# Kernel tuning notes

Hardware: AMD Instinct MI355X
Metric: run time of the kernel (lower is better)

The kernel has to match this reference:

```python
import jax, jax.numpy as jnp
import numpy as np

EPS = 1e-6

def _rms_norm(t, g):
    # t: [B, S, C] (applied before the view to heads, matching the torch code)
    y = t.astype(jnp.float32)
    y = jax.lax.rsqrt(jnp.mean(y * y, axis=-1, keepdims=True) + EPS)
    return (t * y * g).astype(t.dtype)

def _apply_rope(t, cos, sin):
    # t: [B, S, N, D]; cos/sin: [1, S, 1, D//2]; interleaved pair rotation
    b, s, n, d = t.shape
    tr = t.reshape(b, s, n, d // 2, 2)
    tre, tim = tr[..., 0], tr[..., 1]
    out = jnp.stack([tre * cos - tim * sin, tre * sin + tim * cos], axis=-1)
    return out.reshape(b, s, n, d)

def setup_inputs() -> dict:
    key = jax.random.key(0)
    ks = jax.random.split(key, 8)
    B, S, DIM, N, D = 2, 1024, 3072, 24, 128
    x = jax.random.normal(ks[0], (B, S, DIM), dtype=jnp.float32)
    seq_lens = jax.random.randint(ks[1], (B,), S // 2, S + 1, dtype=jnp.int32)
    grid_sizes = jnp.tile(jnp.array([[16, 8, 8]], dtype=jnp.int32), (B, 1))
    # rope angle table [1024, D//2]: pos * inv_freq
    inv_freq = 1.0 / (10000.0 ** (jnp.arange(D // 2, dtype=jnp.float32) * 2.0 / D))
    freqs = jnp.arange(1024, dtype=jnp.float32)[:, None] * inv_freq[None, :]
    sc = 1.0 / np.sqrt(DIM)
    Wq = jax.random.normal(ks[2], (DIM, DIM), dtype=jnp.float32) * sc
    Wk = jax.random.normal(ks[3], (DIM, DIM), dtype=jnp.float32) * sc
    Wv = jax.random.normal(ks[4], (DIM, DIM), dtype=jnp.float32) * sc
    Wo = jax.random.normal(ks[5], (DIM, DIM), dtype=jnp.float32) * sc
    bq = jnp.zeros((DIM,), jnp.float32); bk = jnp.zeros((DIM,), jnp.float32)
    bv = jnp.zeros((DIM,), jnp.float32); bo = jnp.zeros((DIM,), jnp.float32)
    gq = jnp.ones((DIM,), jnp.float32); gk = jnp.ones((DIM,), jnp.float32)
    return {"x": x, "seq_lens": seq_lens, "grid_sizes": grid_sizes, "freqs": freqs,
            "Wq": Wq, "bq": bq, "Wk": Wk, "bk": bk, "Wv": Wv, "bv": bv,
            "Wo": Wo, "bo": bo, "gq": gq, "gk": gk}

def reference(x, seq_lens, grid_sizes, freqs, Wq, bq, Wk, bk, Wv, bv, Wo, bo, gq, gk):
    b, s, dim = x.shape
    d = 2 * freqs.shape[1]          # head_dim
    n = dim // d                    # num_heads
    q = _rms_norm(x @ Wq.T + bq, gq).reshape(b, s, n, d)
    k = _rms_norm(x @ Wk.T + bk, gk).reshape(b, s, n, d)
    v = (x @ Wv.T + bv).reshape(b, s, n, d)
    ang = freqs[:s]                 # [S, D//2]
    cos = jnp.cos(ang)[None, :, None, :]
    sin = jnp.sin(ang)[None, :, None, :]
    q = _apply_rope(q, cos, sin)
    k = _apply_rope(k, cos, sin)
    # full attention (window_size = (-1,-1)), varlen key masking via seq_lens
    scale = d ** -0.5
    scores = jnp.einsum('bind,bjnd->bnij', q, k) * scale   # [B,N,S,S]
    key_valid = jnp.arange(s)[None, :] < seq_lens[:, None]  # [B,S]
    scores = jnp.where(key_valid[:, None, None, :], scores, jnp.finfo(scores.dtype).min)
    p = jax.nn.softmax(scores, axis=-1)
    out = jnp.einsum('bnij,bjnd->bind', p, v).reshape(b, s, dim)
    return out @ Wo.T + bo
```

## Files before the change

kernel.cpp:

```cpp
#include <hip/hip_runtime.h>
#include <cmath>

#define BB   2
#define SS   1024
#define DIMM 3072
#define NHH  24
#define HDD  128
#define MM   (BB * SS)

typedef _Float16 f16;
typedef __attribute__((ext_vector_type(8))) _Float16 half8;
typedef __attribute__((ext_vector_type(4))) float floatx4;
typedef unsigned int u32;
typedef const __attribute__((address_space(1))) u32* gp1;
typedef __attribute__((address_space(3))) u32* lp3;

__device__ __forceinline__ void gload_lds16(const void* g, void* l) {
    __builtin_amdgcn_global_load_lds((gp1)g, (lp3)l, 16, 0, 0);
}

__global__ __launch_bounds__(256) void cvt_f16_kernel(
    const float* __restrict__ in, f16* __restrict__ outp, int n8)
{
    int i = blockIdx.x * 256 + threadIdx.x;
    if (i >= n8) return;
    const float4* p = (const float4*)(in + (size_t)i * 8);
    float4 a = p[0], b = p[1];
    half8 h = {(f16)a.x, (f16)a.y, (f16)a.z, (f16)a.w,
               (f16)b.x, (f16)b.y, (f16)b.z, (f16)b.w};
    *(half8*)(outp + (size_t)i * 8) = h;
}

__global__ __launch_bounds__(256) void cvt3_f16_kernel(
    const float* __restrict__ w0, const float* __restrict__ w1,
    const float* __restrict__ w2, f16* __restrict__ outp, int n8each)
{
    int i = blockIdx.x * 256 + threadIdx.x;
    int sel = i / n8each;
    int j = i - sel * n8each;
    const float* in = sel == 0 ? w0 : (sel == 1 ? w1 : w2);
    const float4* p = (const float4*)(in + (size_t)j * 8);
    float4 a = p[0], b = p[1];
    half8 h = {(f16)a.x, (f16)a.y, (f16)a.z, (f16)a.w,
               (f16)b.x, (f16)b.y, (f16)b.z, (f16)b.w};
    *(half8*)(outp + (size_t)i * 8) = h;
}

__global__ __launch_bounds__(256) void cvt5_f16_kernel(
    const float* __restrict__ x,
    const float* __restrict__ w0, const float* __restrict__ w1,
    const float* __restrict__ w2, const float* __restrict__ w3,
    f16* __restrict__ outx, f16* __restrict__ outw, int n8x, int n8each)
{
    int i = blockIdx.x * 256 + threadIdx.x;
    const float* src;
    f16* op;
    if (i < n8x) {
        src = x + (size_t)i * 8;
        op  = outx + (size_t)i * 8;
    } else {
        int k = i - n8x;
        int sel = k / n8each;
        int j = k - sel * n8each;
        const float* in = sel == 0 ? w0 : (sel == 1 ? w1 : (sel == 2 ? w2 : w3));
        src = in + (size_t)j * 8;
        op  = outw + (size_t)k * 8;
    }
    const float4* p = (const float4*)src;
    float4 a = p[0], b = p[1];
    half8 h = {(f16)a.x, (f16)a.y, (f16)a.z, (f16)a.w,
               (f16)b.x, (f16)b.y, (f16)b.z, (f16)b.w};
    *(half8*)op = h;
}

template<bool QKV>
__global__ __launch_bounds__(256) void gemm_p32(
    const f16* __restrict__ A,
    const f16* __restrict__ W0, const f16* __restrict__ W1, const f16* __restrict__ W2,
    const float* __restrict__ b0, const float* __restrict__ b1, const float* __restrict__ b2,
    f16* __restrict__ D0, f16* __restrict__ D1, f16* __restrict__ D2,
    float* __restrict__ F, const int* __restrict__ seq)
{
    constexpr int K = DIMM;
    constexpr int NSTEP = K / 32;
    constexpr int TS = 128 * 32;
    __shared__ __align__(16) f16 As[3][TS];
    __shared__ __align__(16) f16 Bs[3][TS];

    const int tid  = threadIdx.x;
    const int lane = tid & 63;
    const int wave = tid >> 6;
    const int wm = wave >> 1, wn = wave & 1;
    const int lr = lane & 15;
    const int lq = lane >> 4;

    const int id  = blockIdx.x;
    const int cpx = (int)gridDim.x >> 3;
    const int swz = (id & 7) * cpx + (id >> 3);
    const int bm = (swz & 15) << 7;
    const int bn = (swz >> 4) << 7;

    const f16* Wh; const float* bias; f16* D = nullptr;
    int nloc = bn;
    if constexpr (QKV) {
        int sel = bn / DIMM;
        nloc = bn - sel * DIMM;
        Wh   = sel == 0 ? W0 : (sel == 1 ? W1 : W2);
        bias = sel == 0 ? b0 : (sel == 1 ? b1 : b2);
        D    = sel == 0 ? D0 : (sel == 1 ? D1 : D2);
        if (sel > 0) {
            const int batch  = bm >> 10;
            const int sstart = bm & 1023;
            if (sstart >= seq[batch]) return;
        }
    } else { Wh = W0; bias = b0; }

    const int r0 = tid >> 2;
    const int g0 = ((tid & 3) ^ ((r0 >> 1) & 3)) << 3;
    const int r1 = (tid + 256) >> 2;
    const int g1 = ((tid & 3) ^ ((r1 >> 1) & 3)) << 3;
    const f16* a0  = A  + (size_t)(bm   + r0) * K + g0;
    const f16* a1  = A  + (size_t)(bm   + r1) * K + g1;
    const f16* w0p = Wh + (size_t)(nloc + r0) * K + g0;
    const f16* w1p = Wh + (size_t)(nloc + r1) * K + g1;

    auto STAGE = [&](int t, int buf) {
        const int k0 = t * 32;
        gload_lds16(a0  + k0, &As[buf][(size_t)tid * 8]);
        gload_lds16(a1  + k0, &As[buf][(size_t)(tid + 256) * 8]);
        gload_lds16(w0p + k0, &Bs[buf][(size_t)tid * 8]);
        gload_lds16(w1p + k0, &Bs[buf][(size_t)(tid + 256) * 8]);
    };

    floatx4 acc[4][4];
#pragma unroll
    for (int i = 0; i < 4; ++i)
#pragma unroll
        for (int j = 0; j < 4; ++j) acc[i][j] = (floatx4){0.f, 0.f, 0.f, 0.f};

    auto COMPUTE = [&](int buf) {
        const f16* Ab = &As[buf][0];
        const f16* Bb = &Bs[buf][0];
        half8 af[4], bf[4];
#pragma unroll
        for (int i = 0; i < 4; ++i) {
            int ra = wm * 64 + i * 16 + lr;
            int rb = wn * 64 + i * 16 + lr;
            af[i] = *(const half8*)&Ab[ra * 32 + ((lq ^ ((ra >> 1) & 3)) << 3)];
            bf[i] = *(const half8*)&Bb[rb * 32 + ((lq ^ ((rb >> 1) & 3)) << 3)];
        }
#pragma unroll
        for (int mi = 0; mi < 4; ++mi)
#pragma unroll
            for (int ni = 0; ni < 4; ++ni)
                acc[mi][ni] = __builtin_amdgcn_mfma_f32_16x16x32_f16(af[mi], bf[ni], acc[mi][ni], 0, 0, 0);
    };

    STAGE(0, 0);
    STAGE(1, 1);
    asm volatile("s_waitcnt vmcnt(4)" ::: "memory");
    __builtin_amdgcn_s_barrier();

    int cur = 0, stg = 2;
    for (int ks = 0; ks < NSTEP; ++ks) {
        const bool more = (ks + 2 < NSTEP);
        if (more) STAGE(ks + 2, stg);
        COMPUTE(cur);
        if (more) asm volatile("s_waitcnt vmcnt(4)" ::: "memory");
        else      asm volatile("s_waitcnt vmcnt(0)" ::: "memory");
        __builtin_amdgcn_s_barrier();
        cur = (cur == 2) ? 0 : cur + 1;
        stg = (stg == 2) ? 0 : stg + 1;
    }

    const int crow0 = bm + wm * 64 + (lq << 2);
    const int ccol0 = nloc + wn * 64;
#pragma unroll
    for (int ni = 0; ni < 4; ++ni) {
        const int col = ccol0 + ni * 16 + lr;
        const float bv = bias[col];
#pragma unroll
        for (int mi = 0; mi < 4; ++mi) {
            const int row = crow0 + mi * 16;
#pragma unroll
            for (int r2 = 0; r2 < 4; ++r2) {
                if constexpr (QKV)
                    D[(size_t)(row + r2) * DIMM + col] = (f16)(acc[mi][ni][r2] + bv);
                else
                    F[(size_t)(row + r2) * DIMM + col] = acc[mi][ni][r2] + bv;
            }
        }
    }
}

template<bool QKV>
__global__ __launch_bounds__(256) void gemm_f16m(
    const f16* __restrict__ A,
    const float* __restrict__ W0, const float* __restrict__ W1, const float* __restrict__ W2,
    const float* __restrict__ b0, const float* __restrict__ b1, const float* __restrict__ b2,
    f16* __restrict__ D0, f16* __restrict__ D1, f16* __restrict__ D2,
    float* __restrict__ F)
{
    constexpr int K = DIMM;
    constexpr int NSTEP = K / 32;
    __shared__ f16 As[128 * 32];
    __shared__ f16 Bs[128 * 32];

    const int tid  = threadIdx.x;
    const int lane = tid & 63;
    const int wave = tid >> 6;
    const int wm = wave >> 1, wn = wave & 1;
    const int lr = lane & 15;
    const int lq = lane >> 4;

    const int id  = blockIdx.x;
    const int cpx = (int)gridDim.x >> 3;
    const int swz = (id & 7) * cpx + (id >> 3);
    const int bm = (swz & 15) << 7;
    const int bn = (swz >> 4) << 7;

    const float* W; const float* bias; f16* D = nullptr;
    int nloc = bn;
    if constexpr (QKV) {
        int sel = bn / DIMM;
        nloc = bn - sel * DIMM;
        W    = sel == 0 ? W0 : (sel == 1 ? W1 : W2);
        bias = sel == 0 ? b0 : (sel == 1 ? b1 : b2);
        D    = sel == 0 ? D0 : (sel == 1 ? D1 : D2);
    } else { W = W0; bias = b0; }

    const int r0 = tid >> 2;
    const int c8 = (tid & 3) << 3;
    const float* bp0 = W + (size_t)(nloc + r0) * K + c8;
    const float* bp1 = W + (size_t)(nloc + r0 + 64) * K + c8;

    const int arow_l = lane >> 2;
    const int acol_l = (lane & 3) << 3;
    const f16* agbase = A + (size_t)bm * K;

    float4 sb00, sb01, sb10, sb11;
    auto LOADB = [&](int k0) {
        sb00 = *(const float4*)(bp0 + k0); sb01 = *(const float4*)(bp0 + k0 + 4);
        sb10 = *(const float4*)(bp1 + k0); sb11 = *(const float4*)(bp1 + k0 + 4);
    };
    auto STOREB = [&]() {
        half8 h0 = {(f16)sb00.x, (f16)sb00.y, (f16)sb00.z, (f16)sb00.w,
                    (f16)sb01.x, (f16)sb01.y, (f16)sb01.z, (f16)sb01.w};
        half8 h1 = {(f16)sb10.x, (f16)sb10.y, (f16)sb10.z, (f16)sb10.w,
                    (f16)sb11.x, (f16)sb11.y, (f16)sb11.z, (f16)sb11.w};
        *(half8*)&Bs[r0 * 32 + c8]        = h0;
        *(half8*)&Bs[(r0 + 64) * 32 + c8] = h1;
    };

    floatx4 acc[4][4];
#pragma unroll
    for (int i = 0; i < 4; ++i)
#pragma unroll
        for (int j = 0; j < 4; ++j) acc[i][j] = (floatx4){0.f, 0.f, 0.f, 0.f};

    LOADB(0);
    for (int ks = 0; ks < NSTEP; ++ks) {
        const int k0 = ks * 32;
        __syncthreads();
#pragma unroll
        for (int i = 0; i < 2; ++i) {
            int rbase = wave * 32 + i * 16;
            gload_lds16(agbase + (size_t)(rbase + arow_l) * K + k0 + acol_l,
                        &As[rbase * 32]);
        }
        STOREB();
        __syncthreads();
        if (ks + 1 < NSTEP) LOADB(k0 + 32);

        half8 af[4], bf[4];
#pragma unroll
        for (int i = 0; i < 4; ++i) {
            af[i] = *(const half8*)&As[(wm * 64 + i * 16 + lr) * 32 + lq * 8];
            bf[i] = *(const half8*)&Bs[(wn * 64 + i * 16 + lr) * 32 + lq * 8];
        }
#pragma unroll
        for (int mi = 0; mi < 4; ++mi)
#pragma unroll
            for (int ni = 0; ni < 4; ++ni)
                acc[mi][ni] = __builtin_amdgcn_mfma_f32_16x16x32_f16(af[mi], bf[ni], acc[mi][ni], 0, 0, 0);
    }

    const int crow0 = bm + wm * 64 + (lq << 2);
    const int ccol0 = nloc + wn * 64;
#pragma unroll
    for (int ni = 0; ni < 4; ++ni) {
        const int col = ccol0 + ni * 16 + lr;
        const float bv = bias[col];
#pragma unroll
        for (int mi = 0; mi < 4; ++mi) {
            const int row = crow0 + mi * 16;
#pragma unroll
            for (int r2 = 0; r2 < 4; ++r2) {
                if constexpr (QKV)
                    D[(size_t)(row + r2) * DIMM + col] = (f16)(acc[mi][ni][r2] + bv);
                else
                    F[(size_t)(row + r2) * DIMM + col] = acc[mi][ni][r2] + bv;
            }
        }
    }
}

__global__ __launch_bounds__(192) void rmsnorm_rope_f16(
    f16* __restrict__ q, f16* __restrict__ k,
    const float* __restrict__ gq, const float* __restrict__ gk,
    const float* __restrict__ freqs, const int* __restrict__ seq)
{
    const int row = blockIdx.x;
    const int s = row & (SS - 1);
    if (blockIdx.y == 1 && s >= seq[row >> 10]) return;
    f16* t = (blockIdx.y == 0) ? q : k;
    const float* g = (blockIdx.y == 0) ? gq : gk;
    const int tid = threadIdx.x;
    f16* base = t + (size_t)row * DIMM + tid * 16;

    half8 v0 = *(const half8*)base;
    half8 v1 = *(const half8*)(base + 8);
    float v[16];
#pragma unroll
    for (int j = 0; j < 8; ++j) { v[j] = (float)v0[j]; v[8 + j] = (float)v1[j]; }

    float ssq = 0.f;
#pragma unroll
    for (int j = 0; j < 16; ++j) ssq += v[j] * v[j];
#pragma unroll
    for (int off = 32; off > 0; off >>= 1) ssq += __shfl_down(ssq, off, 64);
    __shared__ float red[3];
    if ((tid & 63) == 0) red[tid >> 6] = ssq;
    __syncthreads();
    float tot = red[0] + red[1] + red[2];
    float sc = rsqrtf(tot * (1.0f / (float)DIMM) + 1e-6f);

    const float* gp = g + tid * 16;
    float y[16];
#pragma unroll
    for (int j = 0; j < 16; ++j) y[j] = v[j] * sc * gp[j];

#pragma unroll
    for (int p = 0; p < 8; ++p) {
        int idx = tid * 16 + 2 * p;
        int f = (idx & 127) >> 1;
        float ang = freqs[s * 64 + f];
        float cc = cosf(ang), sn = sinf(ang);
        float e = y[2 * p], o = y[2 * p + 1];
        y[2 * p]     = e * cc - o * sn;
        y[2 * p + 1] = e * sn + o * cc;
    }
    half8 o0, o1;
#pragma unroll
    for (int j = 0; j < 8; ++j) { o0[j] = (f16)y[j]; o1[j] = (f16)y[8 + j]; }
    *(half8*)base       = o0;
    *(half8*)(base + 8) = o1;
}

__global__ __launch_bounds__(256) void flash_attn_f16(
    const f16* __restrict__ Q, const f16* __restrict__ K,
    const f16* __restrict__ V, const int* __restrict__ seq_lens,
    f16* __restrict__ O)
{
    __shared__ __align__(16) f16 QPs[64 * 128];
    __shared__ __align__(16) f16 Ks[64 * 128];
    __shared__ __align__(16) f16 Vt[128 * 64];

    const int tid  = threadIdx.x;
    const int lane = tid & 63;
    const int wave = tid >> 6;
    const int ln = lane & 15;
    const int lq = lane >> 4;
    const int i0 = blockIdx.x * 64;
    const int h  = blockIdx.y;
    const int b  = blockIdx.z;
    const int slen = seq_lens[b];
    const float scale = 0.08838834764831845f;
    const size_t gstride = NHH * HDD;

    const f16* Qg = Q + ((size_t)(b * SS + i0) * NHH + h) * HDD;
#pragma unroll
    for (int rep = 0; rep < 4; ++rep) {
        int u = tid + rep * 256;
        int r = u >> 4, d0 = (u & 15) << 3;
        half8 qv = *(const half8*)(Qg + (size_t)r * gstride + d0);
        *(half8*)(QPs + r * 128 + (d0 ^ ((r & 7) << 3))) = qv;
    }
    __syncthreads();

    half8 qfrag[4];
    {
        int rq = wave * 16 + ln;
#pragma unroll
        for (int ks = 0; ks < 4; ++ks)
            qfrag[ks] = *(const half8*)(QPs + rq * 128 + ((ks * 32 + lq * 8) ^ ((rq & 7) << 3)));
    }

    floatx4 accO[8];
#pragma unroll
    for (int dt = 0; dt < 8; ++dt) accO[dt] = (floatx4){0.f, 0.f, 0.f, 0.f};
    float mrow[4] = {-3.0e38f, -3.0e38f, -3.0e38f, -3.0e38f};
    float lrow[4] = {0.f, 0.f, 0.f, 0.f};

    const int nT = (slen + 63) >> 6;
    for (int t = 0; t < nT; ++t) {
        const int j0g = t * 64;
        __syncthreads();

        const f16* Kg = K + ((size_t)(b * SS + j0g) * NHH + h) * HDD;
#pragma unroll
        for (int rep = 0; rep < 4; ++rep) {
            int u = tid + rep * 256;
            int r = u >> 4, d0 = (u & 15) << 3;
            half8 kv = *(const half8*)(Kg + (size_t)r * gstride + d0);
            *(half8*)(Ks + r * 128 + (d0 ^ ((r & 7) << 3))) = kv;
        }
        const f16* Vg = V + ((size_t)(b * SS + j0g) * NHH + h) * HDD;
        const half8 zero8 = {(f16)0, (f16)0, (f16)0, (f16)0, (f16)0, (f16)0, (f16)0, (f16)0};
#pragma unroll
        for (int rep = 0; rep < 2; ++rep) {
            int u = tid + rep * 256;
            int jp = u & 31, j0 = jp * 2;
            int d0 = (u >> 5) << 3;
            half8 va = *(const half8*)(Vg + (size_t)j0 * gstride + d0);
            half8 vb = *(const half8*)(Vg + (size_t)(j0 + 1) * gstride + d0);
            if (j0g + j0     >= slen) va = zero8;
            if (j0g + j0 + 1 >= slen) vb = zero8;
#pragma unroll
            for (int i = 0; i < 8; ++i) {
                int d = d0 + i;
                union { f16 h[2]; u32 w; } pk;
                pk.h[0] = va[i]; pk.h[1] = vb[i];
                *(u32*)(Vt + d * 64 + (j0 ^ ((d & 7) << 3))) = pk.w;
            }
        }
        __syncthreads();

        floatx4 acc_s[4];
#pragma unroll
        for (int nt = 0; nt < 4; ++nt) {
            acc_s[nt] = (floatx4){0.f, 0.f, 0.f, 0.f};
            int rk = nt * 16 + ln;
#pragma unroll
            for (int ks = 0; ks < 4; ++ks) {
                half8 kf = *(const half8*)(Ks + rk * 128 + ((ks * 32 + lq * 8) ^ ((rk & 7) << 3)));
                acc_s[nt] = __builtin_amdgcn_mfma_f32_16x16x32_f16(qfrag[ks], kf, acc_s[nt], 0, 0, 0);
            }
        }

        float s[4][4];
#pragma unroll
        for (int nt = 0; nt < 4; ++nt) {
            int j = j0g + nt * 16 + ln;
            bool valid = (j < slen);
#pragma unroll
            for (int r = 0; r < 4; ++r)
                s[nt][r] = valid ? acc_s[nt][r] * scale : -3.0e38f;
        }
        float fct[4];
#pragma unroll
        for (int r = 0; r < 4; ++r) {
            float m4 = fmaxf(fmaxf(s[0][r], s[1][r]), fmaxf(s[2][r], s[3][r]));
            m4 = fmaxf(m4, __shfl_xor(m4, 1, 64));
            m4 = fmaxf(m4, __shfl_xor(m4, 2, 64));
            m4 = fmaxf(m4, __shfl_xor(m4, 4, 64));
            m4 = fmaxf(m4, __shfl_xor(m4, 8, 64));
            float mn = fmaxf(mrow[r], m4);
            fct[r] = __expf(mrow[r] - mn);
            mrow[r] = mn;
            float ls = 0.f;
#pragma unroll
            for (int nt = 0; nt < 4; ++nt) {
                float p = __expf(s[nt][r] - mn);
                s[nt][r] = p;
                ls += p;
            }
            ls += __shfl_xor(ls, 1, 64);
            ls += __shfl_xor(ls, 2, 64);
            ls += __shfl_xor(ls, 4, 64);
            ls += __shfl_xor(ls, 8, 64);
            lrow[r] = lrow[r] * fct[r] + ls;
        }

#pragma unroll
        for (int nt = 0; nt < 4; ++nt) {
#pragma unroll
            for (int r = 0; r < 4; ++r) {
                int rw = lq * 4 + r;
                int j = nt * 16 + ln;
                QPs[(wave * 16 + rw) * 128 + (j ^ ((rw & 7) << 3))] = (f16)s[nt][r];
            }
        }

#pragma unroll
        for (int dt = 0; dt < 8; ++dt)
#pragma unroll
            for (int r = 0; r < 4; ++r) accO[dt][r] *= fct[r];

        half8 pfrag[2];
#pragma unroll
        for (int js = 0; js < 2; ++js)
            pfrag[js] = *(const half8*)(QPs + (wave * 16 + ln) * 128 + ((js * 32 + lq * 8) ^ ((ln & 7) << 3)));
#pragma unroll
        for (int dt = 0; dt < 8; ++dt) {
            int d = dt * 16 + ln;
#pragma unroll
            for (int js = 0; js < 2; ++js) {
                half8 vf = *(const half8*)(Vt + d * 64 + ((js * 32 + lq * 8) ^ ((d & 7) << 3)));
                accO[dt] = __builtin_amdgcn_mfma_f32_16x16x32_f16(pfrag[js], vf, accO[dt], 0, 0, 0);
            }
        }
    }

    float linv[4];
#pragma unroll
    for (int r = 0; r < 4; ++r) linv[r] = 1.0f / lrow[r];
    f16* Og = O + ((size_t)(b * SS + i0) * NHH + h) * HDD;
#pragma unroll
    for (int dt = 0; dt < 8; ++dt) {
#pragma unroll
        for (int r = 0; r < 4; ++r) {
            int qr = wave * 16 + lq * 4 + r;
            int d = dt * 16 + ln;
            Og[(size_t)qr * gstride + d] = (f16)(accO[dt][r] * linv[r]);
        }
    }
}

extern "C" void kernel_launch(void* const* d_in, const int* in_sizes, int n_in,
                              void* d_out, int out_size, void* d_ws, size_t ws_size,
                              hipStream_t stream)
{
    const float* x     = (const float*)d_in[0];
    const int*   seq   = (const int*)d_in[1];
    const float* freqs = (const float*)d_in[3];
    const float* Wq    = (const float*)d_in[4];
    const float* bq    = (const float*)d_in[5];
    const float* Wk    = (const float*)d_in[6];
    const float* bk    = (const float*)d_in[7];
    const float* Wv    = (const float*)d_in[8];
    const float* bv    = (const float*)d_in[9];
    const float* Wo    = (const float*)d_in[10];
    const float* bo    = (const float*)d_in[11];
    const float* gq    = (const float*)d_in[12];
    const float* gk    = (const float*)d_in[13];

    float* out = (float*)d_out;
    const size_t MD = (size_t)MM * DIMM;
    const size_t WD = (size_t)DIMM * DIMM;

    f16* X16 = (f16*)d_ws;
    f16* q16 = X16 + MD;
    f16* k16 = X16 + 2 * MD;
    f16* v16 = (f16*)d_out;

    const int nMD8 = (int)(MD / 8);
    const int nWD8 = (int)(WD / 8);
    const size_t need1 = (3 * MD + 3 * WD) * sizeof(f16);
    const size_t need2 = (3 * MD + 4 * WD) * sizeof(f16);

    if (ws_size >= need2) {
        f16* Wq16 = X16 + 3 * MD;
        f16* Wk16 = Wq16 + WD;
        f16* Wv16 = Wk16 + WD;
        f16* Wo16 = Wv16 + WD;
        cvt5_f16_kernel<<<(nMD8 + 4 * nWD8 + 255) / 256, 256, 0, stream>>>(
            x, Wq, Wk, Wv, Wo, X16, Wq16, nMD8, nWD8);
        gemm_p32<true><<<(MM / 128) * (3 * DIMM / 128), 256, 0, stream>>>(
            X16, Wq16, Wk16, Wv16, bq, bk, bv, q16, k16, v16, nullptr, seq);
        rmsnorm_rope_f16<<<dim3(MM, 2), 192, 0, stream>>>(q16, k16, gq, gk, freqs, seq);
        flash_attn_f16<<<dim3(SS / 64, NHH, BB), 256, 0, stream>>>(q16, k16, v16, seq, X16);
        gemm_p32<false><<<(MM / 128) * (DIMM / 128), 256, 0, stream>>>(
            X16, Wo16, nullptr, nullptr, bo, nullptr, nullptr, nullptr, nullptr, nullptr, out, nullptr);
    } else if (ws_size >= need1) {
        f16* Wq16 = X16 + 3 * MD;
        f16* Wk16 = Wq16 + WD;
        f16* Wv16 = Wk16 + WD;
        f16* Wo16 = Wq16;
        cvt_f16_kernel<<<nMD8 / 256, 256, 0, stream>>>(x, X16, nMD8);
        cvt3_f16_kernel<<<3 * nWD8 / 256, 256, 0, stream>>>(Wq, Wk, Wv, Wq16, nWD8);
        gemm_p32<true><<<(MM / 128) * (3 * DIMM / 128), 256, 0, stream>>>(
            X16, Wq16, Wk16, Wv16, bq, bk, bv, q16, k16, v16, nullptr, seq);
        cvt_f16_kernel<<<nWD8 / 256, 256, 0, stream>>>(Wo, Wo16, nWD8);
        rmsnorm_rope_f16<<<dim3(MM, 2), 192, 0, stream>>>(q16, k16, gq, gk, freqs, seq);
        flash_attn_f16<<<dim3(SS / 64, NHH, BB), 256, 0, stream>>>(q16, k16, v16, seq, X16);
        gemm_p32<false><<<(MM / 128) * (DIMM / 128), 256, 0, stream>>>(
            X16, Wo16, nullptr, nullptr, bo, nullptr, nullptr, nullptr, nullptr, nullptr, out, nullptr);
    } else {
        cvt_f16_kernel<<<nMD8 / 256, 256, 0, stream>>>(x, X16, nMD8);
        gemm_f16m<true><<<(MM / 128) * (3 * DIMM / 128), 256, 0, stream>>>(
            X16, Wq, Wk, Wv, bq, bk, bv, q16, k16, v16, nullptr);
        rmsnorm_rope_f16<<<dim3(MM, 2), 192, 0, stream>>>(q16, k16, gq, gk, freqs, seq);
        flash_attn_f16<<<dim3(SS / 64, NHH, BB), 256, 0, stream>>>(q16, k16, v16, seq, X16);
        gemm_f16m<false><<<(MM / 128) * (DIMM / 128), 256, 0, stream>>>(
            X16, Wo, nullptr, nullptr, bo, nullptr, nullptr, nullptr, nullptr, nullptr, out);
    }
}
```

Baseline: 342.1 us.

## Split-K the output projection GEMM into two halves plus a reduce kernel

Replaces the single output-projection GEMM (384 tiles of 128x128) with a split-K variant that launches 768 blocks, each covering half of K. The first half writes to the output with bias and the second half writes to a float scratch buffer that reuses the Wq16 workspace. A separate kernel then adds the partial into the output. The aim is better CU occupancy on the 256-CU device, at the cost of an extra fp32 write and read of the full output plus one more kernel launch.

```diff
diff --git a/kernel.cpp b/kernel.cpp
--- a/kernel.cpp
+++ b/kernel.cpp
@@ -73,6 +73,17 @@
     *(half8*)op = h;
 }
 
+__global__ __launch_bounds__(256) void reduce_add_kernel(
+    float* __restrict__ out, const float* __restrict__ P, int n4)
+{
+    int i = blockIdx.x * 256 + threadIdx.x;
+    if (i >= n4) return;
+    float4 o = ((const float4*)out)[i];
+    float4 p = ((const float4*)P)[i];
+    o.x += p.x; o.y += p.y; o.z += p.z; o.w += p.w;
+    ((float4*)out)[i] = o;
+}
+
 template<bool QKV>
 __global__ __launch_bounds__(256) void gemm_p32(
     const f16* __restrict__ A,
@@ -189,6 +200,108 @@
                 else
                     F[(size_t)(row + r2) * DIMM + col] = acc[mi][ni][r2] + bv;
             }
+        }
+    }
+}
+
+__global__ __launch_bounds__(256) void gemm_wo_sk(
+    const f16* __restrict__ A, const f16* __restrict__ W,
+    const float* __restrict__ bias, float* __restrict__ out, float* __restrict__ P)
+{
+    constexpr int K = DIMM;
+    constexpr int KH = K / 2;
+    constexpr int NSTEP = KH / 32;
+    constexpr int TS = 128 * 32;
+    __shared__ __align__(16) f16 As[3][TS];
+    __shared__ __align__(16) f16 Bs[3][TS];
+
+    const int tid  = threadIdx.x;
+    const int lane = tid & 63;
+    const int wave = tid >> 6;
+    const int wm = wave >> 1, wn = wave & 1;
+    const int lr = lane & 15;
+    const int lq = lane >> 4;
+
+    const int id  = blockIdx.x;
+    const int cpx = (int)gridDim.x >> 3;
+    const int swz = (id & 7) * cpx + (id >> 3);
+    const int tile = swz >> 1;
+    const int half = swz & 1;
+    const int bm = (tile & 15) << 7;
+    const int bn = (tile >> 4) << 7;
+    const int kbase = half * KH;
+
+    const int r0 = tid >> 2;
+    const int g0 = ((tid & 3) ^ ((r0 >> 1) & 3)) << 3;
+    const int r1 = (tid + 256) >> 2;
+    const int g1 = ((tid & 3) ^ ((r1 >> 1) & 3)) << 3;
+    const f16* a0  = A + (size_t)(bm + r0) * K + kbase + g0;
+    const f16* a1  = A + (size_t)(bm + r1) * K + kbase + g1;
+    const f16* w0p = W + (size_t)(bn + r0) * K + kbase + g0;
+    const f16* w1p = W + (size_t)(bn + r1) * K + kbase + g1;
+
+    auto STAGE = [&](int t, int buf) {
+        const int k0 = t * 32;
+        gload_lds16(a0  + k0, &As[buf][(size_t)tid * 8]);
+        gload_lds16(a1  + k0, &As[buf][(size_t)(tid + 256) * 8]);
+        gload_lds16(w0p + k0, &Bs[buf][(size_t)tid * 8]);
+        gload_lds16(w1p + k0, &Bs[buf][(size_t)(tid + 256) * 8]);
+    };
+
+    floatx4 acc[4][4];
+#pragma unroll
+    for (int i = 0; i < 4; ++i)
+#pragma unroll
+        for (int j = 0; j < 4; ++j) acc[i][j] = (floatx4){0.f, 0.f, 0.f, 0.f};
+
+    auto COMPUTE = [&](int buf) {
+        const f16* Ab = &As[buf][0];
+        const f16* Bb = &Bs[buf][0];
+        half8 af[4], bf[4];
+#pragma unroll
+        for (int i = 0; i < 4; ++i) {
+            int ra = wm * 64 + i * 16 + lr;
+            int rb = wn * 64 + i * 16 + lr;
+            af[i] = *(const half8*)&Ab[ra * 32 + ((lq ^ ((ra >> 1) & 3)) << 3)];
+            bf[i] = *(const half8*)&Bb[rb * 32 + ((lq ^ ((rb >> 1) & 3)) << 3)];
+        }
+#pragma unroll
+        for (int mi = 0; mi < 4; ++mi)
+#pragma unroll
+            for (int ni = 0; ni < 4; ++ni)
+                acc[mi][ni] = __builtin_amdgcn_mfma_f32_16x16x32_f16(af[mi], bf[ni], acc[mi][ni], 0, 0, 0);
+    };
+
+    STAGE(0, 0);
+    STAGE(1, 1);
+    asm volatile("s_waitcnt vmcnt(4)" ::: "memory");
+    __builtin_amdgcn_s_barrier();
+
+    int cur = 0, stg = 2;
+    for (int ks = 0; ks < NSTEP; ++ks) {
+        const bool more = (ks + 2 < NSTEP);
+        if (more) STAGE(ks + 2, stg);
+        COMPUTE(cur);
+        if (more) asm volatile("s_waitcnt vmcnt(4)" ::: "memory");
+        else      asm volatile("s_waitcnt vmcnt(0)" ::: "memory");
+        __builtin_amdgcn_s_barrier();
+        cur = (cur == 2) ? 0 : cur + 1;
+        stg = (stg == 2) ? 0 : stg + 1;
+    }
+
+    const int crow0 = bm + wm * 64 + (lq << 2);
+    const int ccol0 = bn + wn * 64;
+    float* dst = (half == 0) ? out : P;
+#pragma unroll
+    for (int ni = 0; ni < 4; ++ni) {
+        const int col = ccol0 + ni * 16 + lr;
+        const float bv = (half == 0) ? bias[col] : 0.f;
+#pragma unroll
+        for (int mi = 0; mi < 4; ++mi) {
+            const int row = crow0 + mi * 16;
+#pragma unroll
+            for (int r2 = 0; r2 < 4; ++r2)
+                dst[(size_t)(row + r2) * DIMM + col] = acc[mi][ni][r2] + bv;
         }
     }
 }
@@ -564,14 +677,16 @@
         f16* Wk16 = Wq16 + WD;
         f16* Wv16 = Wk16 + WD;
         f16* Wo16 = Wv16 + WD;
+        float* Pws = (float*)Wq16;
         cvt5_f16_kernel<<<(nMD8 + 4 * nWD8 + 255) / 256, 256, 0, stream>>>(
             x, Wq, Wk, Wv, Wo, X16, Wq16, nMD8, nWD8);
         gemm_p32<true><<<(MM / 128) * (3 * DIMM / 128), 256, 0, stream>>>(
             X16, Wq16, Wk16, Wv16, bq, bk, bv, q16, k16, v16, nullptr, seq);
         rmsnorm_rope_f16<<<dim3(MM, 2), 192, 0, stream>>>(q16, k16, gq, gk, freqs, seq);
         flash_attn_f16<<<dim3(SS / 64, NHH, BB), 256, 0, stream>>>(q16, k16, v16, seq, X16);
-        gemm_p32<false><<<(MM / 128) * (DIMM / 128), 256, 0, stream>>>(
-            X16, Wo16, nullptr, nullptr, bo, nullptr, nullptr, nullptr, nullptr, nullptr, out, nullptr);
+        gemm_wo_sk<<<2 * (MM / 128) * (DIMM / 128), 256, 0, stream>>>(
+            X16, Wo16, bo, out, Pws);
+        reduce_add_kernel<<<(int)(MD / 4 / 256), 256, 0, stream>>>(out, Pws, (int)(MD / 4));
     } else if (ws_size >= need1) {
         f16* Wq16 = X16 + 3 * MD;
         f16* Wk16 = Wq16 + WD;
```

Result: no change. 342.8 us (+0.2%).
